# Kernel tuning notes

Hardware: AMD Instinct MI355X
Metric: run time of the kernel (lower is better)

Reference implementation:

```python
import jax, jax.numpy as jnp
import numpy as np

NUM_NODES = 100000
NODE_CH = 3     # node_fiber_channels (degree-0)
EDGE_CH = 3     # edge_fiber_channels (degree-0)
MID = 32        # RadialProfile hidden dim (NVIDIA SE3-Transformer default)
VALUE_CH = 1    # fiber_out channels // channels_div = 3 // 2
KQ_CH = 1       # key/query channels (match value fiber on shared degrees)
BATCH = 64


def setup_inputs() -> dict:
    key = jax.random.key(0)
    ks = jax.random.split(key, 8)
    s = 0.1
    return {
        "input_data": jax.random.normal(ks[0], (BATCH, 3, NUM_NODES, 3), jnp.float32),
        # RadialProfile MLP: edge_feats -> MID -> MID -> (VALUE_CH+KQ_CH)*NODE_CH (last layer no bias)
        "W1": jax.random.normal(ks[1], (EDGE_CH, MID), jnp.float32) * s,
        "b1": jnp.zeros((MID,), jnp.float32),
        "W2": jax.random.normal(ks[2], (MID, MID), jnp.float32) * s,
        "b2": jnp.zeros((MID,), jnp.float32),
        "W3": jax.random.normal(ks[3], (MID, (VALUE_CH + KQ_CH) * NODE_CH), jnp.float32) * s,
        # LinearSE3 query (deg 0): (KQ_CH, NODE_CH)
        "Wq": jax.random.normal(ks[4], (KQ_CH, NODE_CH), jnp.float32) * s,
        # LinearSE3 project after cat-skip: (NODE_CH, VALUE_CH + NODE_CH)
        "Wp": jax.random.normal(ks[5], (NODE_CH, VALUE_CH + NODE_CH), jnp.float32) * s,
    }


def reference(input_data, W1, b1, W2, b2, W3, Wq, Wp):
    B, C, N, _ = input_data.shape
    node = input_data[:, 0]               # (B, N, 3) degree-0 node feats
    edge = input_data[:, 2]               # (B, E=N, 3) degree-0 edge feats
    src = jnp.arange(N)                   # ring graph: i -> (i+1) % N
    dst = (src + 1) % N

    # ConvSE3 deg0->deg0 (to_key_value): radial MLP on invariant edge feats
    # produces a per-edge (out_ch, in_ch) matrix applied to source-node feats.
    h = jax.nn.relu(edge @ W1 + b1)
    h = jax.nn.relu(h @ W2 + b2)
    R = (h @ W3).reshape(B, N, VALUE_CH + KQ_CH, NODE_CH)      # (B,E,2,3)
    kv = jnp.einsum('beoc,bec->beo', R, node[:, src])          # (B,E,2)
    value = kv[..., 0]                                         # chunk: value first
    key_e = kv[..., 1]                                         # key second

    # LinearSE3 query at nodes
    q = jnp.einsum('bnc,kc->bnk', node, Wq)[..., 0]            # (B,N)

    # AttentionSE3: dot(key, query[dst]) / sqrt(key feats), softmax over
    # incoming edges of each destination node (ring: exactly one per node).
    logits = key_e * q[:, dst] / jnp.sqrt(jnp.float32(KQ_CH))  # (B,E)
    m = jnp.full((B, N), -jnp.inf, logits.dtype).at[:, dst].max(logits)
    ex = jnp.exp(logits - m[:, dst])
    denom = jnp.zeros((B, N), logits.dtype).at[:, dst].add(ex)
    alpha = ex / denom[:, dst]
    z = jnp.zeros((B, N), logits.dtype).at[:, dst].add(alpha * value)  # (B,N)

    # aggregate_residual 'cat' ([attn_out, node]) then LinearSE3 project
    feat = jnp.concatenate([z[..., None], node], axis=-1)      # (B,N,4)
    out0 = jnp.einsum('bnc,oc->bno', feat, Wp)                 # (B,N,3)

    # channels 1 and 2 pass through unchanged
    return input_data.at[:, 0].set(out0)
```

## Files before the change

### kernel.cpp

```cpp
#include <hip/hip_runtime.h>

#define N_NODES 100000
#define BATCH   64
#define MID     32
#define LSTRIDE 80
#define WLDS    (64 * LSTRIDE)
#define TOTAL   (BATCH * N_NODES)
#define CHF     (N_NODES * 3)

typedef __attribute__((ext_vector_type(2))) __fp16 h2v;
typedef _Float16 __attribute__((ext_vector_type(8))) f16x8;
typedef float __attribute__((ext_vector_type(4))) f32x4;
typedef float __attribute__((ext_vector_type(2))) f32x2;

union H2U  { h2v h; unsigned int u; };
union U4H8 { uint4 u; f16x8 h; };

struct __attribute__((packed, aligned(4))) F4u { f32x4 v; };

typedef f32x4 f32x4a4 __attribute__((aligned(4)));
typedef f32x2 f32x2a4 __attribute__((aligned(4)));

__device__ __forceinline__ void nts4(float* p, f32x4 v) {
    __builtin_nontemporal_store(v, (f32x4a4*)p);
}
__device__ __forceinline__ void nts2(float* p, f32x2 v) {
    __builtin_nontemporal_store(v, (f32x2a4*)p);
}
__device__ __forceinline__ void nts1(float* p, float v) {
    __builtin_nontemporal_store(v, p);
}

__global__ void prep_weights(const float* __restrict__ W1, const float* __restrict__ b1,
                             const float* __restrict__ W2, const float* __restrict__ W3,
                             uint4* __restrict__ wf, unsigned int* __restrict__ aux) {
    int t = threadIdx.x;
    if (t < 128) {
        int grp = t >> 6, l = t & 63;
        int j = (l & 15) + 16 * grp, k0 = (l >> 4) * 8;
        unsigned int pk[4];
#pragma unroll
        for (int m = 0; m < 4; ++m) {
            H2U a; a.h = __builtin_amdgcn_cvt_pkrtz(W2[(k0 + 2*m) * MID + j],
                                                    W2[(k0 + 2*m + 1) * MID + j]);
            pk[m] = a.u;
        }
        wf[t] = make_uint4(pk[0], pk[1], pk[2], pk[3]);
    } else if (t < 192) {
        int l = t & 63;
        int c = l & 15, q4 = l >> 4;
        unsigned int pk[4];
#pragma unroll
        for (int mp = 0; mp < 4; ++mp) {
            int jb = (mp < 2) ? (4*q4 + 2*mp) : (16 + 4*q4 + 2*(mp - 2));
            float x0 = (c < 3) ? W3[jb * 6 + c] : 0.f;
            float x1 = (c < 3) ? W3[(jb + 1) * 6 + c] : 0.f;
            H2U a; a.h = __builtin_amdgcn_cvt_pkrtz(x0, x1);
            pk[mp] = a.u;
        }
        wf[128 + l] = make_uint4(pk[0], pk[1], pk[2], pk[3]);
    } else if (t < 240) {
        int i = t - 192;
        int k = i >> 4, m = i & 15;
        H2U a; a.h = __builtin_amdgcn_cvt_pkrtz(W1[k * MID + 2*m], W1[k * MID + 2*m + 1]);
        aux[i] = a.u;
    } else {
        int m = t - 240;
        H2U a; a.h = __builtin_amdgcn_cvt_pkrtz(b1[2*m], b1[2*m + 1]);
        aux[48 + m] = a.u;
    }
}

__global__ __launch_bounds__(256) void xattn_kernel(
    const float* __restrict__ in,
    const unsigned int* __restrict__ aux,
    const float* __restrict__ b2,
    const uint4* __restrict__ wf,
    const float* __restrict__ Wp,
    float* __restrict__ out)
{
    __shared__ __attribute__((aligned(16))) char ldsbuf[4 * WLDS];
    int tid  = threadIdx.x;
    int lane = tid & 63;
    int wave = tid >> 6;
    char* L  = ldsbuf + wave * WLDS;

    int idx = blockIdx.x * 256 + tid;
    int b = idx / N_NODES;
    int n = idx - b * N_NODES;
    bool last  = (idx == TOTAL - 1);
    bool btail = (n == N_NODES - 1);

    const float* inb  = in  + (size_t)b * 3 * CHF;
    float*       outb = out + (size_t)b * 3 * CHF;

    f32x4 ndv = ((const F4u*)(inb + (size_t)n * 3))->v;
    f32x4 c1v = ((const F4u*)(inb + (size_t)CHF + (size_t)n * 3))->v;
    f32x4 edv;
    const float* e_ptr = inb + (size_t)2 * CHF + (size_t)n * 3;
    if (!last) edv = ((const F4u*)e_ptr)->v;
    else       edv = (f32x4){e_ptr[0], e_ptr[1], e_ptr[2], 0.f};

    float qn0 = ndv.x, qn1 = ndv.y, qn2 = ndv.z;

    {
        float* o1p = outb + (size_t)CHF + (size_t)n * 3;
        nts4(o1p, c1v);
        float* o2p = outb + (size_t)2 * CHF + (size_t)n * 3;
        if (!btail) nts4(o2p, edv);
        else { nts1(o2p, edv.x); nts1(o2p + 1, edv.y); nts1(o2p + 2, edv.z); }
    }

    H2U s0_, s1_, s2_;
    s0_.h = __builtin_amdgcn_cvt_pkrtz(qn0, qn1);
    s1_.h = __builtin_amdgcn_cvt_pkrtz(qn2, edv.x);
    s2_.h = __builtin_amdgcn_cvt_pkrtz(edv.y, edv.z);
    unsigned int t0 = __shfl_up(s0_.u, 1);
    unsigned int t1 = __shfl_up(s1_.u, 1);
    unsigned int t2 = __shfl_up(s2_.u, 1);
    if (lane == 0 || n == 0) {
        int p = (n == 0) ? (N_NODES - 1) : (n - 1);
        const float* np_ = inb + (size_t)p * 3;
        const float* epp = inb + (size_t)2 * CHF + (size_t)p * 3;
        H2U a, bb, c;
        a.h  = __builtin_amdgcn_cvt_pkrtz(np_[0], np_[1]);
        bb.h = __builtin_amdgcn_cvt_pkrtz(np_[2], epp[0]);
        c.h  = __builtin_amdgcn_cvt_pkrtz(epp[1], epp[2]);
        t0 = a.u; t1 = bb.u; t2 = c.u;
    }
    H2U u0, u1, u2; u0.u = t0; u1.u = t1; u2.u = t2;
    float pp0 = (float)u0.h[0], pp1 = (float)u0.h[1], pp2 = (float)u1.h[0];
    h2v eh0 = {u1.h[1], u1.h[1]};
    h2v eh1 = {u2.h[0], u2.h[0]};
    h2v eh2 = {u2.h[1], u2.h[1]};

    h2v zz = {(__fp16)0.0f, (__fp16)0.0f};
    unsigned int hp[16];
#pragma unroll
    for (int m = 0; m < 16; ++m) {
        H2U acc, w0, w1_, w2_;
        acc.u = aux[48 + m];
        w0.u  = aux[m];
        w1_.u = aux[16 + m];
        w2_.u = aux[32 + m];
        acc.h = eh0 * w0.h + acc.h;
        acc.h = eh1 * w1_.h + acc.h;
        acc.h = eh2 * w2_.h + acc.h;
        acc.h = __builtin_elementwise_max(acc.h, zz);
        hp[m] = acc.u;
    }
    {
        uint4* row = (uint4*)(L + lane * LSTRIDE);
        row[0] = make_uint4(hp[0],  hp[1],  hp[2],  hp[3]);
        row[1] = make_uint4(hp[4],  hp[5],  hp[6],  hp[7]);
        row[2] = make_uint4(hp[8],  hp[9],  hp[10], hp[11]);
        row[3] = make_uint4(hp[12], hp[13], hp[14], hp[15]);
    }

    int r16 = lane & 15;
    int q4  = lane >> 4;
    U4H8 wb20; wb20.u = wf[lane];
    U4H8 wb21; wb21.u = wf[64 + lane];
    U4H8 wb3;  wb3.u  = wf[128 + lane];
    f32x4 bi0 = *(const f32x4*)(b2 + 4*q4);
    f32x4 bi1 = *(const f32x4*)(b2 + 16 + 4*q4);

#pragma unroll
    for (int pt = 0; pt < 4; ++pt) {
        U4H8 hB; hB.u = *(const uint4*)(L + (pt*16 + r16) * LSTRIDE + q4 * 16);
        f32x4 acc0 = bi0;
        f32x4 acc1 = bi1;
        acc0 = __builtin_amdgcn_mfma_f32_16x16x32_f16(wb20.h, hB.h, acc0, 0, 0, 0);
        acc1 = __builtin_amdgcn_mfma_f32_16x16x32_f16(wb21.h, hB.h, acc1, 0, 0, 0);

        H2U g0, g1, g2, g3;
        g0.h = __builtin_elementwise_max(__builtin_amdgcn_cvt_pkrtz(acc0[0], acc0[1]), zz);
        g1.h = __builtin_elementwise_max(__builtin_amdgcn_cvt_pkrtz(acc0[2], acc0[3]), zz);
        g2.h = __builtin_elementwise_max(__builtin_amdgcn_cvt_pkrtz(acc1[0], acc1[1]), zz);
        g3.h = __builtin_elementwise_max(__builtin_amdgcn_cvt_pkrtz(acc1[2], acc1[3]), zz);
        U4H8 b3f; b3f.u = make_uint4(g0.u, g1.u, g2.u, g3.u);

        f32x4 c3 = __builtin_amdgcn_mfma_f32_16x16x32_f16(wb3.h, b3f.h,
                                                          (f32x4){0.f,0.f,0.f,0.f}, 0, 0, 0);

        if (q4 == 0) {
            int pos = pt*16 + r16;
            H2U za; za.h = __builtin_amdgcn_cvt_pkrtz(c3[0], c3[1]);
            H2U zb; zb.h = __builtin_amdgcn_cvt_pkrtz(c3[2], 0.f);
            *(uint2*)(L + (pos >> 1) * LSTRIDE + 64 + (pos & 1) * 8) = make_uint2(za.u, zb.u);
        }
    }

    uint2 zr = *(const uint2*)(L + (lane >> 1) * LSTRIDE + 64 + (lane & 1) * 8);
    H2U za, zb; za.u = zr.x; zb.u = zr.y;
    float z = fmaf((float)za.h[0], pp0,
              fmaf((float)za.h[1], pp1, (float)zb.h[0] * pp2));

    float vo[3];
#pragma unroll
    for (int o = 0; o < 3; ++o) {
        float v = Wp[o*4 + 0] * z;
        v = fmaf(Wp[o*4 + 1], qn0, v);
        v = fmaf(Wp[o*4 + 2], qn1, v);
        v = fmaf(Wp[o*4 + 3], qn2, v);
        vo[o] = v;
    }
    float* o0 = outb + (size_t)n * 3;
    nts2(o0, (f32x2){vo[0], vo[1]});
    nts1(o0 + 2, vo[2]);
}

extern "C" void kernel_launch(void* const* d_in, const int* in_sizes, int n_in,
                              void* d_out, int out_size, void* d_ws, size_t ws_size,
                              hipStream_t stream) {
    const float* in = (const float*)d_in[0];
    const float* W1 = (const float*)d_in[1];
    const float* b1 = (const float*)d_in[2];
    const float* W2 = (const float*)d_in[3];
    const float* b2 = (const float*)d_in[4];
    const float* W3 = (const float*)d_in[5];
    const float* Wp = (const float*)d_in[7];
    float* out = (float*)d_out;

    uint4* wf = (uint4*)d_ws;
    unsigned int* aux = (unsigned int*)(wf + 192);
    hipLaunchKernelGGL(prep_weights, dim3(1), dim3(256), 0, stream, W1, b1, W2, W3, wf, aux);

    int blocks = TOTAL / 256;
    hipLaunchKernelGGL(xattn_kernel, dim3(blocks), dim3(256), 0, stream,
                       in, aux, b2, wf, Wp, out);
}
```

Baseline: 80.49 us.

## Move first radial MLP layer onto MFMA and shrink LDS staging

The first radial-profile layer (3->32) moves from per-lane packed fp16 FMAs plus an LDS row write onto an MFMA with a zero-padded K dimension. Edge features are broadcast across lanes with shuffles, and the layer-2 B operand comes straight from layer-1 registers. LDS is cut to a small per-wave buffer that only holds the final kv values, which should raise occupancy and remove the LDS round trip. The cost is two extra MFMAs per 16-position tile, extra shuffles and more weight registers, mostly wasted on zero padding.

```diff
diff --git a/kernel.cpp b/kernel.cpp
--- a/kernel.cpp
+++ b/kernel.cpp
@@ -3,8 +3,6 @@
 #define N_NODES 100000
 #define BATCH   64
 #define MID     32
-#define LSTRIDE 80
-#define WLDS    (64 * LSTRIDE)
 #define TOTAL   (BATCH * N_NODES)
 #define CHF     (N_NODES * 3)
 
@@ -20,35 +18,40 @@
 
 typedef f32x4 f32x4a4 __attribute__((aligned(4)));
 typedef f32x2 f32x2a4 __attribute__((aligned(4)));
-
-__device__ __forceinline__ void nts4(float* p, f32x4 v) {
-    __builtin_nontemporal_store(v, (f32x4a4*)p);
-}
-__device__ __forceinline__ void nts2(float* p, f32x2 v) {
-    __builtin_nontemporal_store(v, (f32x2a4*)p);
-}
-__device__ __forceinline__ void nts1(float* p, float v) {
-    __builtin_nontemporal_store(v, p);
-}
-
-__global__ void prep_weights(const float* __restrict__ W1, const float* __restrict__ b1,
-                             const float* __restrict__ W2, const float* __restrict__ W3,
-                             uint4* __restrict__ wf, unsigned int* __restrict__ aux) {
+__device__ __forceinline__ void nts4(float* p, f32x4 v) { __builtin_nontemporal_store(v, (f32x4a4*)p); }
+__device__ __forceinline__ void nts2(float* p, f32x2 v) { __builtin_nontemporal_store(v, (f32x2a4*)p); }
+__device__ __forceinline__ void nts1(float* p, float v) { __builtin_nontemporal_store(v, p); }
+
+__global__ void prep_weights(const float* __restrict__ W1, const float* __restrict__ W2,
+                             const float* __restrict__ W3, uint4* __restrict__ wf) {
     int t = threadIdx.x;
+    if (t >= 320) return;
+    int l = t & 63;
+    int q4 = l >> 4;
     if (t < 128) {
-        int grp = t >> 6, l = t & 63;
-        int j = (l & 15) + 16 * grp, k0 = (l >> 4) * 8;
+        int tile = t >> 6;
+        int j = (l & 15) + 16 * tile;
+        unsigned int pk0 = 0, pk1 = 0;
+        if (q4 == 0) {
+            H2U a; a.h = __builtin_amdgcn_cvt_pkrtz(W1[0 * MID + j], W1[1 * MID + j]);
+            H2U b; b.h = __builtin_amdgcn_cvt_pkrtz(W1[2 * MID + j], 0.f);
+            pk0 = a.u; pk1 = b.u;
+        }
+        wf[t] = make_uint4(pk0, pk1, 0u, 0u);
+    } else if (t < 256) {
+        int tt = t - 128;
+        int tile = tt >> 6;
+        int j2 = (l & 15) + 16 * tile;
         unsigned int pk[4];
 #pragma unroll
-        for (int m = 0; m < 4; ++m) {
-            H2U a; a.h = __builtin_amdgcn_cvt_pkrtz(W2[(k0 + 2*m) * MID + j],
-                                                    W2[(k0 + 2*m + 1) * MID + j]);
-            pk[m] = a.u;
-        }
-        wf[t] = make_uint4(pk[0], pk[1], pk[2], pk[3]);
-    } else if (t < 192) {
-        int l = t & 63;
-        int c = l & 15, q4 = l >> 4;
+        for (int mp = 0; mp < 4; ++mp) {
+            int jb = (mp < 2) ? (4*q4 + 2*mp) : (16 + 4*q4 + 2*(mp - 2));
+            H2U a; a.h = __builtin_amdgcn_cvt_pkrtz(W2[jb * MID + j2], W2[(jb + 1) * MID + j2]);
+            pk[mp] = a.u;
+        }
+        wf[128 + tt] = make_uint4(pk[0], pk[1], pk[2], pk[3]);
+    } else {
+        int c = l & 15;
         unsigned int pk[4];
 #pragma unroll
         for (int mp = 0; mp < 4; ++mp) {
@@ -58,32 +61,23 @@
             H2U a; a.h = __builtin_amdgcn_cvt_pkrtz(x0, x1);
             pk[mp] = a.u;
         }
-        wf[128 + l] = make_uint4(pk[0], pk[1], pk[2], pk[3]);
-    } else if (t < 240) {
-        int i = t - 192;
-        int k = i >> 4, m = i & 15;
-        H2U a; a.h = __builtin_amdgcn_cvt_pkrtz(W1[k * MID + 2*m], W1[k * MID + 2*m + 1]);
-        aux[i] = a.u;
-    } else {
-        int m = t - 240;
-        H2U a; a.h = __builtin_amdgcn_cvt_pkrtz(b1[2*m], b1[2*m + 1]);
-        aux[48 + m] = a.u;
+        wf[256 + l] = make_uint4(pk[0], pk[1], pk[2], pk[3]);
     }
 }
 
 __global__ __launch_bounds__(256) void xattn_kernel(
     const float* __restrict__ in,
-    const unsigned int* __restrict__ aux,
+    const float* __restrict__ b1,
     const float* __restrict__ b2,
     const uint4* __restrict__ wf,
     const float* __restrict__ Wp,
     float* __restrict__ out)
 {
-    __shared__ __attribute__((aligned(16))) char ldsbuf[4 * WLDS];
+    __shared__ __attribute__((aligned(16))) char ldsbuf[4 * 512];
     int tid  = threadIdx.x;
     int lane = tid & 63;
     int wave = tid >> 6;
-    char* L  = ldsbuf + wave * WLDS;
+    char* ZB = ldsbuf + wave * 512;
 
     int idx = blockIdx.x * 256 + tid;
     int b = idx / N_NODES;
@@ -130,68 +124,61 @@
     }
     H2U u0, u1, u2; u0.u = t0; u1.u = t1; u2.u = t2;
     float pp0 = (float)u0.h[0], pp1 = (float)u0.h[1], pp2 = (float)u1.h[0];
-    h2v eh0 = {u1.h[1], u1.h[1]};
-    h2v eh1 = {u2.h[0], u2.h[0]};
-    h2v eh2 = {u2.h[1], u2.h[1]};
-
-    h2v zz = {(__fp16)0.0f, (__fp16)0.0f};
-    unsigned int hp[16];
-#pragma unroll
-    for (int m = 0; m < 16; ++m) {
-        H2U acc, w0, w1_, w2_;
-        acc.u = aux[48 + m];
-        w0.u  = aux[m];
-        w1_.u = aux[16 + m];
-        w2_.u = aux[32 + m];
-        acc.h = eh0 * w0.h + acc.h;
-        acc.h = eh1 * w1_.h + acc.h;
-        acc.h = eh2 * w2_.h + acc.h;
-        acc.h = __builtin_elementwise_max(acc.h, zz);
-        hp[m] = acc.u;
-    }
-    {
-        uint4* row = (uint4*)(L + lane * LSTRIDE);
-        row[0] = make_uint4(hp[0],  hp[1],  hp[2],  hp[3]);
-        row[1] = make_uint4(hp[4],  hp[5],  hp[6],  hp[7]);
-        row[2] = make_uint4(hp[8],  hp[9],  hp[10], hp[11]);
-        row[3] = make_uint4(hp[12], hp[13], hp[14], hp[15]);
-    }
+    unsigned int epk0 = __builtin_amdgcn_alignbit(u2.u, u1.u, 16);
+    unsigned int epk1 = u2.u >> 16;
 
     int r16 = lane & 15;
     int q4  = lane >> 4;
-    U4H8 wb20; wb20.u = wf[lane];
-    U4H8 wb21; wb21.u = wf[64 + lane];
-    U4H8 wb3;  wb3.u  = wf[128 + lane];
-    f32x4 bi0 = *(const f32x4*)(b2 + 4*q4);
-    f32x4 bi1 = *(const f32x4*)(b2 + 16 + 4*q4);
+    U4H8 w1a0; w1a0.u = wf[lane];
+    U4H8 w1a1; w1a1.u = wf[64 + lane];
+    U4H8 w2a0; w2a0.u = wf[128 + lane];
+    U4H8 w2a1; w2a1.u = wf[192 + lane];
+    U4H8 w3a;  w3a.u  = wf[256 + lane];
+    f32x4 b1i0 = *(const f32x4*)(b1 + 4*q4);
+    f32x4 b1i1 = *(const f32x4*)(b1 + 16 + 4*q4);
+    f32x4 b2i0 = *(const f32x4*)(b2 + 4*q4);
+    f32x4 b2i1 = *(const f32x4*)(b2 + 16 + 4*q4);
+    h2v zz = {(__fp16)0.0f, (__fp16)0.0f};
 
 #pragma unroll
     for (int pt = 0; pt < 4; ++pt) {
-        U4H8 hB; hB.u = *(const uint4*)(L + (pt*16 + r16) * LSTRIDE + q4 * 16);
-        f32x4 acc0 = bi0;
-        f32x4 acc1 = bi1;
-        acc0 = __builtin_amdgcn_mfma_f32_16x16x32_f16(wb20.h, hB.h, acc0, 0, 0, 0);
-        acc1 = __builtin_amdgcn_mfma_f32_16x16x32_f16(wb21.h, hB.h, acc1, 0, 0, 0);
+        unsigned int e0f = __shfl(epk0, pt*16 + r16);
+        unsigned int e1f = __shfl(epk1, pt*16 + r16);
+        U4H8 b1f; b1f.u = make_uint4(q4 == 0 ? e0f : 0u, q4 == 0 ? e1f : 0u, 0u, 0u);
+
+        f32x4 a0 = b1i0, a1 = b1i1;
+        a0 = __builtin_amdgcn_mfma_f32_16x16x32_f16(w1a0.h, b1f.h, a0, 0, 0, 0);
+        a1 = __builtin_amdgcn_mfma_f32_16x16x32_f16(w1a1.h, b1f.h, a1, 0, 0, 0);
 
         H2U g0, g1, g2, g3;
-        g0.h = __builtin_elementwise_max(__builtin_amdgcn_cvt_pkrtz(acc0[0], acc0[1]), zz);
-        g1.h = __builtin_elementwise_max(__builtin_amdgcn_cvt_pkrtz(acc0[2], acc0[3]), zz);
-        g2.h = __builtin_elementwise_max(__builtin_amdgcn_cvt_pkrtz(acc1[0], acc1[1]), zz);
-        g3.h = __builtin_elementwise_max(__builtin_amdgcn_cvt_pkrtz(acc1[2], acc1[3]), zz);
-        U4H8 b3f; b3f.u = make_uint4(g0.u, g1.u, g2.u, g3.u);
-
-        f32x4 c3 = __builtin_amdgcn_mfma_f32_16x16x32_f16(wb3.h, b3f.h,
+        g0.h = __builtin_elementwise_max(__builtin_amdgcn_cvt_pkrtz(a0[0], a0[1]), zz);
+        g1.h = __builtin_elementwise_max(__builtin_amdgcn_cvt_pkrtz(a0[2], a0[3]), zz);
+        g2.h = __builtin_elementwise_max(__builtin_amdgcn_cvt_pkrtz(a1[0], a1[1]), zz);
+        g3.h = __builtin_elementwise_max(__builtin_amdgcn_cvt_pkrtz(a1[2], a1[3]), zz);
+        U4H8 b2f; b2f.u = make_uint4(g0.u, g1.u, g2.u, g3.u);
+
+        f32x4 c0 = b2i0, c1 = b2i1;
+        c0 = __builtin_amdgcn_mfma_f32_16x16x32_f16(w2a0.h, b2f.h, c0, 0, 0, 0);
+        c1 = __builtin_amdgcn_mfma_f32_16x16x32_f16(w2a1.h, b2f.h, c1, 0, 0, 0);
+
+        H2U k0, k1, k2, k3;
+        k0.h = __builtin_elementwise_max(__builtin_amdgcn_cvt_pkrtz(c0[0], c0[1]), zz);
+        k1.h = __builtin_elementwise_max(__builtin_amdgcn_cvt_pkrtz(c0[2], c0[3]), zz);
+        k2.h = __builtin_elementwise_max(__builtin_amdgcn_cvt_pkrtz(c1[0], c1[1]), zz);
+        k3.h = __builtin_elementwise_max(__builtin_amdgcn_cvt_pkrtz(c1[2], c1[3]), zz);
+        U4H8 b3f; b3f.u = make_uint4(k0.u, k1.u, k2.u, k3.u);
+
+        f32x4 c3 = __builtin_amdgcn_mfma_f32_16x16x32_f16(w3a.h, b3f.h,
                                                           (f32x4){0.f,0.f,0.f,0.f}, 0, 0, 0);
 
         if (q4 == 0) {
-            int pos = pt*16 + r16;
             H2U za; za.h = __builtin_amdgcn_cvt_pkrtz(c3[0], c3[1]);
             H2U zb; zb.h = __builtin_amdgcn_cvt_pkrtz(c3[2], 0.f);
-            *(uint2*)(L + (pos >> 1) * LSTRIDE + 64 + (pos & 1) * 8) = make_uint2(za.u, zb.u);
-        }
-    }
-
-    uint2 zr = *(const uint2*)(L + (lane >> 1) * LSTRIDE + 64 + (lane & 1) * 8);
+            *(uint2*)(ZB + (pt*16 + r16) * 8) = make_uint2(za.u, zb.u);
+        }
+    }
+
+    uint2 zr = *(const uint2*)(ZB + lane * 8);
     H2U za, zb; za.u = zr.x; zb.u = zr.y;
     float z = fmaf((float)za.h[0], pp0,
               fmaf((float)za.h[1], pp1, (float)zb.h[0] * pp2));
@@ -223,10 +210,9 @@
     float* out = (float*)d_out;
 
     uint4* wf = (uint4*)d_ws;
-    unsigned int* aux = (unsigned int*)(wf + 192);
-    hipLaunchKernelGGL(prep_weights, dim3(1), dim3(256), 0, stream, W1, b1, W2, W3, wf, aux);
+    hipLaunchKernelGGL(prep_weights, dim3(1), dim3(320), 0, stream, W1, W2, W3, wf);
 
     int blocks = TOTAL / 256;
     hipLaunchKernelGGL(xattn_kernel, dim3(blocks), dim3(256), 0, stream,
-                       in, aux, b2, wf, Wp, out);
+                       in, b1, b2, wf, Wp, out);
 }
```

Result: slower. 82.76 us (+2.8%).
